# Kernel optimization log

Measured on AMD Instinct MI355X. Metric: run time of the kernel, lower is better.

The kernel has to match this reference:

```python
import jax, jax.numpy as jnp
import numpy as np

B, L, C, K = 8, 16384, 64, 7
NORM_FACTOR = 1.0
LN_EPS = 1e-6


def setup_inputs() -> dict:
    key = jax.random.key(0)
    k0, k1, k2 = jax.random.split(key, 3)
    x = jax.random.normal(k0, (B, L, C), dtype=jnp.float32)
    # lecun_normal-style init for (C_out, C_in, K) dynamic-conv weights
    weights = jax.random.normal(k1, (C, C, K), dtype=jnp.float32) / np.float32(np.sqrt(C))
    ln_scale = jnp.ones((C,), dtype=jnp.float32)
    ln_bias = jnp.zeros((C,), dtype=jnp.float32)
    conv_kernel = jax.random.normal(k2, (C, C), dtype=jnp.float32) / np.float32(np.sqrt(C))
    conv_bias = jnp.zeros((C,), dtype=jnp.float32)
    prelu_slope = jnp.asarray(0.01, dtype=jnp.float32)
    return {"x": x, "weights": weights, "ln_scale": ln_scale, "ln_bias": ln_bias,
            "conv_kernel": conv_kernel, "conv_bias": conv_bias, "prelu_slope": prelu_slope}


def reference(x, weights, ln_scale, ln_bias, conv_kernel, conv_bias, prelu_slope):
    b, l, c = x.shape
    k = weights.shape[-1]
    x0 = x  # residual source, (B, L, C)

    # im2col unfold over sequence: window 2K, stride 2, no padding
    p = jax.lax.conv_general_dilated_patches(
        jnp.transpose(x, (0, 2, 1)),  # (B, C, L)
        filter_shape=(2 * k,), window_strides=(2,), padding=((0, 0),))
    t = p.shape[-1]  # out_len = (L - 2K)//2 + 1
    p = jnp.reshape(p, (b, c, 2 * k, t))
    p = jnp.transpose(p, (0, 1, 3, 2))  # (B, C, T, 2K)

    # dynamic weights from the trailing 2T inputs: (B, 2T, C) x (C, C, K) -> (B, C, 2T, K)
    w = jnp.einsum('blc,dck->bdlk', x0[:, -(t * 2):, :], weights)
    even_seq = w[:, :, ::2, :]   # (B, C, T, K)
    odd_seq = w[:, :, 1::2, :]   # (B, C, T, K)
    w = jnp.stack([even_seq, odd_seq], axis=-1)         # (B, C, T, K, 2)
    w = jnp.reshape(w, (b, c, t, k * 2))                # interleaved (B, C, T, 2K)
    w = jnp.tanh(w / NORM_FACTOR)

    # gated windowed sum
    y = jnp.sum(p * w, axis=3)          # (B, C, T)
    y = jnp.transpose(y, (0, 2, 1))     # (B, T, C)

    # inner skip: stride-2 subsample of input, aligned to the tail
    y = x0[:, ::2, :][:, -t:, :] + y

    # LayerNorm over channel dim (flax default eps=1e-6, with scale and bias)
    mu = jnp.mean(y, axis=-1, keepdims=True)
    var = jnp.mean(jnp.square(y - mu), axis=-1, keepdims=True)
    yn = (y - mu) * jax.lax.rsqrt(var + LN_EPS) * ln_scale + ln_bias

    # 1x1 conv + PReLU + outer skip
    z = jnp.einsum('btc,co->bto', yn, conv_kernel) + conv_bias
    z = jnp.where(z >= 0, z, prelu_slope * z)
    return yn + z
```

## Files before the change

kernel.cpp:

```cpp
#include <hip/hip_runtime.h>
#include <stdint.h>

#define BB 8
#define LLEN 16384
#define CC 64
#define TOUT 8186
#define TILE_T 32
#define NROWS 76
#define SXS 68
#define YNS 66
#define YNBS 76

typedef __attribute__((ext_vector_type(8))) short short8;
typedef __attribute__((ext_vector_type(4))) float float4v;
typedef __attribute__((ext_vector_type(4))) unsigned short ushort4v;

__device__ inline unsigned short f2bf(float f) {
  union { float f; uint32_t u; } v; v.f = f;
  uint32_t r = v.u + 0x7fffu + ((v.u >> 16) & 1u);
  return (unsigned short)(r >> 16);
}
__device__ inline float rcp_fast(float x) {
  float r; asm("v_rcp_f32 %0, %1" : "=v"(r) : "v"(x)); return r;
}
__device__ inline float exp2_fast(float x) {
  float r; asm("v_exp_f32 %0, %1" : "=v"(r) : "v"(x)); return r;
}
__device__ inline float tanh_fast(float a) {
  float e = exp2_fast(a * 2.885390082f);
  return __builtin_fmaf(-2.0f, rcp_fast(e + 1.0f), 1.0f);
}

__global__ void prep_frags(const float* __restrict__ weights,
                           const float* __restrict__ ck,
                           unsigned short* __restrict__ wfrag,
                           unsigned short* __restrict__ ckfrag)
{
  int bid = blockIdx.x, tid = threadIdx.x;
  if (bid < 56) {
    int nt = bid >> 1, kh = bid & 1;
    for (int e = tid; e < 512; e += 256) {
      int ln = e >> 3, j = e & 7;
      int kk = nt >> 2;
      int d  = (nt & 3) * 16 + (ln & 15);
      int cp = kh * 32 + (ln >> 4) * 8 + j;
      wfrag[(bid * 64 + ln) * 8 + j] = f2bf(weights[d * 448 + cp * 7 + kk]);
    }
  } else {
    int bb2 = bid - 56;
    int nt = bb2 >> 1, kh = bb2 & 1;
    for (int e = tid; e < 512; e += 256) {
      int ln = e >> 3, j = e & 7;
      int oo = nt * 16 + (ln & 15);
      int c2 = kh * 32 + (ln >> 4) * 8 + j;
      ckfrag[(bb2 * 64 + ln) * 8 + j] = f2bf(ck[c2 * 64 + oo]);
    }
  }
}

__global__ __launch_bounds__(256, 6)
void convblock_main(const float* __restrict__ x,
                    const unsigned short* __restrict__ wfrag,
                    const unsigned short* __restrict__ ckfrag,
                    const float* __restrict__ ln_scale,
                    const float* __restrict__ ln_bias,
                    const float* __restrict__ conv_bias,
                    const float* __restrict__ prelu_slope,
                    float* __restrict__ out)
{
  __shared__ __align__(16) char smem[20672];
  float*          sx2 = (float*)smem;
  unsigned short* ynb = (unsigned short*)smem;
  float*          ynf = (float*)(smem + 4864);

  const int tid  = threadIdx.x;
  const int b    = blockIdx.x >> 8;
  const int t0   = (blockIdx.x & 255) * TILE_T;
  const int lane = tid & 63;
  const int w    = tid >> 6;
  const int l15  = tid & 15;
  const int q    = (tid >> 4) & 3;

  {
    const float* xb = x + (size_t)b * ((size_t)LLEN * CC);
    #pragma unroll
    for (int i = 0; i < 5; ++i) {
      int idx = tid + i * 256;
      if (idx < NROWS * 16) {
        int row = idx >> 4, f4 = idx & 15;
        int rowg = 2 * t0 + row;
        if (rowg > LLEN - 1) rowg = LLEN - 1;
        float4v v = *(const float4v*)(xb + (size_t)rowg * CC + f4 * 4);
        int base = row * SXS + 16 * (f4 & 3) + (f4 >> 2);
        sx2[base + 0]  = v[0];
        sx2[base + 4]  = v[1];
        sx2[base + 8]  = v[2];
        sx2[base + 12] = v[3];
      }
    }
  }
  __syncthreads();

  short8 a0, a1;
  {
    const int rowoff = (12 + 16 * w + l15) * SXS;
    #pragma unroll
    for (int j = 0; j < 8; ++j) {
      int c0 = q * 8 + j;
      int w0 = 16 * ((c0 >> 2) & 3) + (c0 >> 4) + 4 * (c0 & 3);
      a0[j] = (short)f2bf(sx2[rowoff + w0]);
      int c1 = 32 + q * 8 + j;
      int w1 = 16 * ((c1 >> 2) & 3) + (c1 >> 4) + 4 * (c1 & 3);
      a1[j] = (short)f2bf(sx2[rowoff + w1]);
    }
  }

  float y[2][4];
  #pragma unroll
  for (int dlt = 0; dlt < 2; ++dlt)
    #pragma unroll
    for (int dq = 0; dq < 4; ++dq) y[dlt][dq] = 0.f;

  const float4v zacc = (float4v){0.f, 0.f, 0.f, 0.f};
  const int dtbase = 8 * w + 2 * q;
  const unsigned short* wp = wfrag + lane * 8;
  #pragma unroll 1
  for (int kk = 0; kk < 7; ++kk) {
    float4v acc[4];
    #pragma unroll
    for (int dq = 0; dq < 4; ++dq) {
      short8 b0 = *(const short8*)(wp + dq * 1024);
      short8 b1 = *(const short8*)(wp + dq * 1024 + 512);
      float4v a = __builtin_amdgcn_mfma_f32_16x16x32_bf16(a0, b0, zacc, 0, 0, 0);
      acc[dq] = __builtin_amdgcn_mfma_f32_16x16x32_bf16(a1, b1, a, 0, 0, 0);
    }
    #pragma unroll
    for (int dlt = 0; dlt < 2; ++dlt) {
      int rowe = 2 * (dtbase + dlt) + 2 * kk;
      float4v xe = *(const float4v*)&sx2[rowe * SXS + l15 * 4];
      float4v xo = *(const float4v*)&sx2[(rowe + 1) * SXS + l15 * 4];
      #pragma unroll
      for (int dq = 0; dq < 4; ++dq) {
        float ge = tanh_fast(acc[dq][2 * dlt + 0]);
        float go = tanh_fast(acc[dq][2 * dlt + 1]);
        y[dlt][dq] += xe[dq] * ge + xo[dq] * go;
      }
    }
    wp += 4096;
  }
  #pragma unroll
  for (int dlt = 0; dlt < 2; ++dlt) {
    int rowe = 2 * (dtbase + dlt) + 12;
    float4v xe = *(const float4v*)&sx2[rowe * SXS + l15 * 4];
    #pragma unroll
    for (int dq = 0; dq < 4; ++dq) y[dlt][dq] += xe[dq];
  }

  float lnS[4], lnB[4];
  #pragma unroll
  for (int dq = 0; dq < 4; ++dq) {
    lnS[dq] = ln_scale[16 * dq + l15];
    lnB[dq] = ln_bias[16 * dq + l15];
  }
  float ynr[2][4];
  #pragma unroll
  for (int dlt = 0; dlt < 2; ++dlt) {
    float s1 = y[dlt][0] + y[dlt][1] + y[dlt][2] + y[dlt][3];
    float s2 = y[dlt][0]*y[dlt][0] + y[dlt][1]*y[dlt][1]
             + y[dlt][2]*y[dlt][2] + y[dlt][3]*y[dlt][3];
    #pragma unroll
    for (int m = 1; m < 16; m <<= 1) {
      s1 += __shfl_xor(s1, m, 64);
      s2 += __shfl_xor(s2, m, 64);
    }
    float mu   = s1 * (1.0f / 64.0f);
    float var  = s2 * (1.0f / 64.0f) - mu * mu;
    float rstd = rsqrtf(var + 1e-6f);
    #pragma unroll
    for (int dq = 0; dq < 4; ++dq)
      ynr[dlt][dq] = (y[dlt][dq] - mu) * rstd * lnS[dq] + lnB[dq];
  }
  __syncthreads();

  #pragma unroll
  for (int dlt = 0; dlt < 2; ++dlt) {
    int dt = dtbase + dlt;
    #pragma unroll
    for (int dq = 0; dq < 4; ++dq) {
      ynf[dt * YNS + 16 * dq + l15] = ynr[dlt][dq];
      ynb[dt * YNBS + 16 * dq + l15] = f2bf(ynr[dlt][dq]);
    }
  }
  __syncthreads();

  const float sl = prelu_slope[0];
  const int   o  = 16 * w + l15;
  const float cb = conv_bias[o];
  short8 bf0 = *(const short8*)&ckfrag[((w * 2 + 0) * 64 + lane) * 8];
  short8 bf1 = *(const short8*)&ckfrag[((w * 2 + 1) * 64 + lane) * 8];
  #pragma unroll
  for (int mt = 0; mt < 2; ++mt) {
    short8 af0 = *(const short8*)&ynb[(mt * 16 + l15) * YNBS + q * 8];
    short8 af1 = *(const short8*)&ynb[(mt * 16 + l15) * YNBS + 32 + q * 8];
    float4v zc = __builtin_amdgcn_mfma_f32_16x16x32_bf16(af0, bf0, zacc, 0, 0, 0);
    zc = __builtin_amdgcn_mfma_f32_16x16x32_bf16(af1, bf1, zc, 0, 0, 0);
    #pragma unroll
    for (int r = 0; r < 4; ++r) {
      int t  = mt * 16 + 4 * q + r;
      int tg = t0 + t;
      if (tg < TOUT) {
        float z = zc[r] + cb;
        z = (z >= 0.f) ? z : sl * z;
        out[((size_t)b * TOUT + tg) * CC + o] = ynf[t * YNS + o] + z;
      }
    }
  }
}

extern "C" void kernel_launch(void* const* d_in, const int* in_sizes, int n_in,
                              void* d_out, int out_size, void* d_ws, size_t ws_size,
                              hipStream_t stream)
{
  const float* x        = (const float*)d_in[0];
  const float* weights  = (const float*)d_in[1];
  const float* ln_scale = (const float*)d_in[2];
  const float* ln_bias  = (const float*)d_in[3];
  const float* ck       = (const float*)d_in[4];
  const float* cb       = (const float*)d_in[5];
  const float* slope    = (const float*)d_in[6];
  unsigned short* wfrag  = (unsigned short*)d_ws;
  unsigned short* ckfrag = (unsigned short*)((char*)d_ws + 57344);

  prep_frags<<<64, 256, 0, stream>>>(weights, ck, wfrag, ckfrag);
  convblock_main<<<BB * 256, 256, 0, stream>>>(x, wfrag, ckfrag, ln_scale,
                                               ln_bias, cb, slope, (float*)d_out);
}
```

Measured before the change: 111.5 us.

## Double time tile per block so each wave reuses weight fragments twice

Doubles the per-block time tile from 32 to 64 outputs, so each wave computes two 16-row MFMA tiles for every weight fragment it loads. This halves global weight-fragment loads per output and reduces the halo overlap of the input rows loaded into shared memory. In exchange, shared memory grows to about 38 KB, register pressure rises (launch bounds drop from 6 to 4 blocks per CU), and the grid halves to 1024 blocks, which lowers occupancy and parallelism.

```diff
diff --git a/kernel.cpp b/kernel.cpp
--- a/kernel.cpp
+++ b/kernel.cpp
@@ -5,8 +5,9 @@
 #define LLEN 16384
 #define CC 64
 #define TOUT 8186
-#define TILE_T 32
-#define NROWS 76
+#define TILE_T 64
+#define NTILES 128
+#define NROWS 140
 #define SXS 68
 #define YNS 66
 #define YNBS 76
@@ -58,7 +59,7 @@
   }
 }
 
-__global__ __launch_bounds__(256, 6)
+__global__ __launch_bounds__(256, 4)
 void convblock_main(const float* __restrict__ x,
                     const unsigned short* __restrict__ wfrag,
                     const unsigned short* __restrict__ ckfrag,
@@ -68,14 +69,14 @@
                     const float* __restrict__ prelu_slope,
                     float* __restrict__ out)
 {
-  __shared__ __align__(16) char smem[20672];
+  __shared__ __align__(16) char smem[38080];
   float*          sx2 = (float*)smem;
   unsigned short* ynb = (unsigned short*)smem;
-  float*          ynf = (float*)(smem + 4864);
+  float*          ynf = (float*)(smem + 9728);
 
   const int tid  = threadIdx.x;
-  const int b    = blockIdx.x >> 8;
-  const int t0   = (blockIdx.x & 255) * TILE_T;
+  const int b    = blockIdx.x >> 7;
+  const int t0   = (blockIdx.x & 127) * TILE_T;
   const int lane = tid & 63;
   const int w    = tid >> 6;
   const int l15  = tid & 15;
@@ -84,7 +85,7 @@
   {
     const float* xb = x + (size_t)b * ((size_t)LLEN * CC);
     #pragma unroll
-    for (int i = 0; i < 5; ++i) {
+    for (int i = 0; i < 9; ++i) {
       int idx = tid + i * 256;
       if (idx < NROWS * 16) {
         int row = idx >> 4, f4 = idx & 15;
@@ -101,60 +102,81 @@
   }
   __syncthreads();
 
-  short8 a0, a1;
+  short8 a0, a1, a2, a3;
   {
-    const int rowoff = (12 + 16 * w + l15) * SXS;
+    const int ro0 = (12 + 32 * w + l15) * SXS;
+    const int ro1 = ro0 + 16 * SXS;
     #pragma unroll
     for (int j = 0; j < 8; ++j) {
       int c0 = q * 8 + j;
       int w0 = 16 * ((c0 >> 2) & 3) + (c0 >> 4) + 4 * (c0 & 3);
-      a0[j] = (short)f2bf(sx2[rowoff + w0]);
       int c1 = 32 + q * 8 + j;
       int w1 = 16 * ((c1 >> 2) & 3) + (c1 >> 4) + 4 * (c1 & 3);
-      a1[j] = (short)f2bf(sx2[rowoff + w1]);
-    }
-  }
-
-  float y[2][4];
-  #pragma unroll
-  for (int dlt = 0; dlt < 2; ++dlt)
-    #pragma unroll
-    for (int dq = 0; dq < 4; ++dq) y[dlt][dq] = 0.f;
+      a0[j] = (short)f2bf(sx2[ro0 + w0]);
+      a1[j] = (short)f2bf(sx2[ro0 + w1]);
+      a2[j] = (short)f2bf(sx2[ro1 + w0]);
+      a3[j] = (short)f2bf(sx2[ro1 + w1]);
+    }
+  }
+
+  float y[2][2][4];
+  #pragma unroll
+  for (int s = 0; s < 2; ++s)
+    #pragma unroll
+    for (int dlt = 0; dlt < 2; ++dlt)
+      #pragma unroll
+      for (int dq = 0; dq < 4; ++dq) y[s][dlt][dq] = 0.f;
 
   const float4v zacc = (float4v){0.f, 0.f, 0.f, 0.f};
-  const int dtbase = 8 * w + 2 * q;
+  const int tb2 = 32 * w + 4 * q;
   const unsigned short* wp = wfrag + lane * 8;
   #pragma unroll 1
   for (int kk = 0; kk < 7; ++kk) {
-    float4v acc[4];
+    float4v acc0[4], acc1[4];
     #pragma unroll
     for (int dq = 0; dq < 4; ++dq) {
       short8 b0 = *(const short8*)(wp + dq * 1024);
       short8 b1 = *(const short8*)(wp + dq * 1024 + 512);
-      float4v a = __builtin_amdgcn_mfma_f32_16x16x32_bf16(a0, b0, zacc, 0, 0, 0);
-      acc[dq] = __builtin_amdgcn_mfma_f32_16x16x32_bf16(a1, b1, a, 0, 0, 0);
-    }
-    #pragma unroll
-    for (int dlt = 0; dlt < 2; ++dlt) {
-      int rowe = 2 * (dtbase + dlt) + 2 * kk;
+      float4v u = __builtin_amdgcn_mfma_f32_16x16x32_bf16(a0, b0, zacc, 0, 0, 0);
+      acc0[dq] = __builtin_amdgcn_mfma_f32_16x16x32_bf16(a1, b1, u, 0, 0, 0);
+      float4v v = __builtin_amdgcn_mfma_f32_16x16x32_bf16(a2, b0, zacc, 0, 0, 0);
+      acc1[dq] = __builtin_amdgcn_mfma_f32_16x16x32_bf16(a3, b1, v, 0, 0, 0);
+    }
+    #pragma unroll
+    for (int dlt = 0; dlt < 2; ++dlt) {
+      int rowe = tb2 + 2 * dlt + 2 * kk;
       float4v xe = *(const float4v*)&sx2[rowe * SXS + l15 * 4];
       float4v xo = *(const float4v*)&sx2[(rowe + 1) * SXS + l15 * 4];
       #pragma unroll
       for (int dq = 0; dq < 4; ++dq) {
-        float ge = tanh_fast(acc[dq][2 * dlt + 0]);
-        float go = tanh_fast(acc[dq][2 * dlt + 1]);
-        y[dlt][dq] += xe[dq] * ge + xo[dq] * go;
+        float ge = tanh_fast(acc0[dq][2 * dlt + 0]);
+        float go = tanh_fast(acc0[dq][2 * dlt + 1]);
+        y[0][dlt][dq] += xe[dq] * ge + xo[dq] * go;
+      }
+    }
+    #pragma unroll
+    for (int dlt = 0; dlt < 2; ++dlt) {
+      int rowe = tb2 + 16 + 2 * dlt + 2 * kk;
+      float4v xe = *(const float4v*)&sx2[rowe * SXS + l15 * 4];
+      float4v xo = *(const float4v*)&sx2[(rowe + 1) * SXS + l15 * 4];
+      #pragma unroll
+      for (int dq = 0; dq < 4; ++dq) {
+        float ge = tanh_fast(acc1[dq][2 * dlt + 0]);
+        float go = tanh_fast(acc1[dq][2 * dlt + 1]);
+        y[1][dlt][dq] += xe[dq] * ge + xo[dq] * go;
       }
     }
     wp += 4096;
   }
   #pragma unroll
-  for (int dlt = 0; dlt < 2; ++dlt) {
-    int rowe = 2 * (dtbase + dlt) + 12;
-    float4v xe = *(const float4v*)&sx2[rowe * SXS + l15 * 4];
-    #pragma unroll
-    for (int dq = 0; dq < 4; ++dq) y[dlt][dq] += xe[dq];
-  }
+  for (int s = 0; s < 2; ++s)
+    #pragma unroll
+    for (int dlt = 0; dlt < 2; ++dlt) {
+      int rowe = tb2 + 16 * s + 2 * dlt + 12;
+      float4v xe = *(const float4v*)&sx2[rowe * SXS + l15 * 4];
+      #pragma unroll
+      for (int dq = 0; dq < 4; ++dq) y[s][dlt][dq] += xe[dq];
+    }
 
   float lnS[4], lnB[4];
   #pragma unroll
@@ -162,35 +184,39 @@
     lnS[dq] = ln_scale[16 * dq + l15];
     lnB[dq] = ln_bias[16 * dq + l15];
   }
-  float ynr[2][4];
-  #pragma unroll
-  for (int dlt = 0; dlt < 2; ++dlt) {
-    float s1 = y[dlt][0] + y[dlt][1] + y[dlt][2] + y[dlt][3];
-    float s2 = y[dlt][0]*y[dlt][0] + y[dlt][1]*y[dlt][1]
-             + y[dlt][2]*y[dlt][2] + y[dlt][3]*y[dlt][3];
-    #pragma unroll
-    for (int m = 1; m < 16; m <<= 1) {
-      s1 += __shfl_xor(s1, m, 64);
-      s2 += __shfl_xor(s2, m, 64);
-    }
-    float mu   = s1 * (1.0f / 64.0f);
-    float var  = s2 * (1.0f / 64.0f) - mu * mu;
-    float rstd = rsqrtf(var + 1e-6f);
-    #pragma unroll
-    for (int dq = 0; dq < 4; ++dq)
-      ynr[dlt][dq] = (y[dlt][dq] - mu) * rstd * lnS[dq] + lnB[dq];
-  }
+  float ynr[2][2][4];
+  #pragma unroll
+  for (int s = 0; s < 2; ++s)
+    #pragma unroll
+    for (int dlt = 0; dlt < 2; ++dlt) {
+      float s1 = y[s][dlt][0] + y[s][dlt][1] + y[s][dlt][2] + y[s][dlt][3];
+      float s2 = y[s][dlt][0]*y[s][dlt][0] + y[s][dlt][1]*y[s][dlt][1]
+               + y[s][dlt][2]*y[s][dlt][2] + y[s][dlt][3]*y[s][dlt][3];
+      #pragma unroll
+      for (int m = 1; m < 16; m <<= 1) {
+        s1 += __shfl_xor(s1, m, 64);
+        s2 += __shfl_xor(s2, m, 64);
+      }
+      float mu   = s1 * (1.0f / 64.0f);
+      float var  = s2 * (1.0f / 64.0f) - mu * mu;
+      float rstd = rsqrtf(var + 1e-6f);
+      #pragma unroll
+      for (int dq = 0; dq < 4; ++dq)
+        ynr[s][dlt][dq] = (y[s][dlt][dq] - mu) * rstd * lnS[dq] + lnB[dq];
+    }
   __syncthreads();
 
   #pragma unroll
-  for (int dlt = 0; dlt < 2; ++dlt) {
-    int dt = dtbase + dlt;
-    #pragma unroll
-    for (int dq = 0; dq < 4; ++dq) {
-      ynf[dt * YNS + 16 * dq + l15] = ynr[dlt][dq];
-      ynb[dt * YNBS + 16 * dq + l15] = f2bf(ynr[dlt][dq]);
-    }
-  }
+  for (int s = 0; s < 2; ++s)
+    #pragma unroll
+    for (int dlt = 0; dlt < 2; ++dlt) {
+      int dt = 16 * w + 8 * s + 2 * q + dlt;
+      #pragma unroll
+      for (int dq = 0; dq < 4; ++dq) {
+        ynf[dt * YNS + 16 * dq + l15] = ynr[s][dlt][dq];
+        ynb[dt * YNBS + 16 * dq + l15] = f2bf(ynr[s][dlt][dq]);
+      }
+    }
   __syncthreads();
 
   const float sl = prelu_slope[0];
@@ -199,7 +225,7 @@
   short8 bf0 = *(const short8*)&ckfrag[((w * 2 + 0) * 64 + lane) * 8];
   short8 bf1 = *(const short8*)&ckfrag[((w * 2 + 1) * 64 + lane) * 8];
   #pragma unroll
-  for (int mt = 0; mt < 2; ++mt) {
+  for (int mt = 0; mt < 4; ++mt) {
     short8 af0 = *(const short8*)&ynb[(mt * 16 + l15) * YNBS + q * 8];
     short8 af1 = *(const short8*)&ynb[(mt * 16 + l15) * YNBS + 32 + q * 8];
     float4v zc = __builtin_amdgcn_mfma_f32_16x16x32_bf16(af0, bf0, zacc, 0, 0, 0);
@@ -232,6 +258,6 @@
   unsigned short* ckfrag = (unsigned short*)((char*)d_ws + 57344);
 
   prep_frags<<<64, 256, 0, stream>>>(weights, ck, wfrag, ckfrag);
-  convblock_main<<<BB * 256, 256, 0, stream>>>(x, wfrag, ckfrag, ln_scale,
-                                               ln_bias, cb, slope, (float*)d_out);
-}
+  convblock_main<<<BB * NTILES, 256, 0, stream>>>(x, wfrag, ckfrag, ln_scale,
+                                                  ln_bias, cb, slope, (float*)d_out);
+}
```

Measured after the change: 111.6 us. No clear change (+0.1%).
